# Kernel optimization log

Measured on AMD Instinct MI355X. Metric: run time of the kernel, lower is better.

## Reference

```python
import jax, jax.numpy as jnp
import numpy as np

# Dims: B batch, C=P channels (features per pixel), H*W=N pixels, M ELM models, Q=1 hidden units
M, Q, B, C, H, W_SP = 4, 1, 32, 1024, 28, 28
P = C
N = H * W_SP
EPS = 1e-10


def _lcg_weights(m, n, seed):
    """Deterministic LCG pseudo-random weights, z-score standardized (ELM_AE init)."""
    L = m * n
    a, b, c = L + 2, L + 3, float(L) ** 2
    v = np.zeros(L, dtype=np.float64)
    v[0] = seed + 1.0
    for i in range(1, L):
        v[i] = (a * v[i - 1] + b) % c
    v = (v - v.mean()) / (v.std() + EPS)
    return v.reshape(m, n).astype(np.float32)


def setup_inputs() -> dict:
    key = jax.random.key(0)
    x = jax.random.normal(key, (B, C, H, W_SP), dtype=jnp.float32)
    # One Q x P random input-weight matrix per ELM model, seed = model * (Q * P)
    Wm = jnp.stack([jnp.asarray(_lcg_weights(Q, P, model * (Q * P))) for model in range(M)])  # [M, Q, P]
    return {"x": x, "Wm": Wm}


def reference(x, Wm):
    b, c, h, w = x.shape
    # _norm('l2', ...): per-channel L2 normalization over (h, w), as F.normalize(dim=(1,2))
    norms = jnp.linalg.norm(x.reshape(b, c, h * w), axis=-1)[:, :, None, None]  # [B, C, 1, 1]
    xn = x / jnp.maximum(norms, EPS)
    X = xn.reshape(b, c, h * w)  # meta activation map per sample: [B, P, N]
    # ELM-AE hidden layer, batched over (sample, model): g = sigmoid(W @ X)
    G = jax.nn.sigmoid(jnp.einsum('mqp,bpn->bmqn', Wm, X))  # [B, M, Q, N]
    # fit_AE: output weights beta = pinv(g^T) @ X^T  -> [Q, P]
    pinvGt = jnp.linalg.pinv(jnp.swapaxes(G, -1, -2))       # [B, M, Q, N]
    beta = jnp.einsum('bmqn,bpn->bmqp', pinvGt, X)          # [B, M, Q, P]
    # sum over the M models; Q == 1 so flatten (Q, P) -> Q*P features
    feats = beta.sum(axis=1).reshape(b, -1)                 # [B, Q*P]
    return jnp.nan_to_num(feats)
```

## Files before the change

### kernel.cpp

```cpp
#include <hip/hip_runtime.h>
#include <math.h>

#define BATCH 32
#define CH    1024
#define NPix  784
#define MMOD  4
#define NPC   32
#define PPC   32
#define T2    832

__device__ __forceinline__ float wave_reduce(float s) {
    #pragma unroll
    for (int off = 32; off; off >>= 1) s += __shfl_down(s, off, 64);
    return s;
}

__device__ __forceinline__ float dpp_wave_sum(float v) {
    int x;
    x = __builtin_amdgcn_update_dpp(0, __builtin_bit_cast(int, v), 0x111, 0xf, 0xf, true);
    v += __builtin_bit_cast(float, x);
    x = __builtin_amdgcn_update_dpp(0, __builtin_bit_cast(int, v), 0x112, 0xf, 0xf, true);
    v += __builtin_bit_cast(float, x);
    x = __builtin_amdgcn_update_dpp(0, __builtin_bit_cast(int, v), 0x114, 0xf, 0xf, true);
    v += __builtin_bit_cast(float, x);
    x = __builtin_amdgcn_update_dpp(0, __builtin_bit_cast(int, v), 0x118, 0xf, 0xf, true);
    v += __builtin_bit_cast(float, x);
    x = __builtin_amdgcn_update_dpp(0, __builtin_bit_cast(int, v), 0x142, 0xa, 0xf, true);
    v += __builtin_bit_cast(float, x);
    x = __builtin_amdgcn_update_dpp(0, __builtin_bit_cast(int, v), 0x143, 0xc, 0xf, true);
    v += __builtin_bit_cast(float, x);
    return v;
}

__global__ __launch_bounds__(T2) void k_nz(const float* __restrict__ x,
                                           const float* __restrict__ Wm,
                                           float* __restrict__ inv_norm,
                                           float* __restrict__ zpart) {
    __shared__ float sq_l[PPC * 13];
    __shared__ float4 wl4[PPC];
    const int blk = blockIdx.x;
    const int b  = blk >> 5;
    const int pc = blk & (NPC - 1);
    const int t = threadIdx.x;
    const int wv = t >> 6, lane = t & 63;
    const bool act = (t < NPix);
    const float* xb = x + ((size_t)b * CH + (size_t)pc * PPC) * NPix;
    const float* xp = xb + (act ? t : 0);

    float xv[PPC];
    #pragma unroll
    for (int pp = 0; pp < PPC; pp++) xv[pp] = xp[(size_t)pp * NPix];
    if (!act) {
        #pragma unroll
        for (int pp = 0; pp < PPC; pp++) xv[pp] = 0.f;
    }

    #pragma unroll
    for (int pp = 0; pp < PPC; pp++) {
        float s = dpp_wave_sum(xv[pp] * xv[pp]);
        if (lane == 63) sq_l[pp * 13 + wv] = s;
    }
    __syncthreads();

    if (t < PPC) {
        float s = 0.f;
        #pragma unroll
        for (int w = 0; w < 13; w++) s += sq_l[t * 13 + w];
        const float inv = 1.f / fmaxf(sqrtf(s), 1e-10f);
        const int p = pc * PPC + t;
        inv_norm[b * CH + p] = inv;
        float4 w4;
        w4.x = Wm[0 * CH + p] * inv;
        w4.y = Wm[1 * CH + p] * inv;
        w4.z = Wm[2 * CH + p] * inv;
        w4.w = Wm[3 * CH + p] * inv;
        wl4[t] = w4;
    }
    __syncthreads();

    if (act) {
        float a0 = 0.f, a1 = 0.f, a2 = 0.f, a3 = 0.f;
        #pragma unroll
        for (int pp = 0; pp < PPC; pp++) {
            float4 w = wl4[pp];
            a0 += w.x * xv[pp];
            a1 += w.y * xv[pp];
            a2 += w.z * xv[pp];
            a3 += w.w * xv[pp];
        }
        size_t base = ((size_t)blk * MMOD) * NPix + t;
        zpart[base]            = a0;
        zpart[base + NPix]     = a1;
        zpart[base + 2 * NPix] = a2;
        zpart[base + 3 * NPix] = a3;
    }
}

__global__ __launch_bounds__(T2) void k_gh(const float* __restrict__ zpart,
                                           float* __restrict__ h) {
    __shared__ float red[13][MMOD];
    __shared__ float s2s[MMOD];
    const int b = blockIdx.x;
    const int t = threadIdx.x;
    const int wv = t >> 6, lane = t & 63;
    const bool act = (t < NPix);

    float g[MMOD];
    #pragma unroll
    for (int m = 0; m < MMOD; m++) {
        float z = 0.f;
        if (act) {
            #pragma unroll 8
            for (int pc = 0; pc < NPC; pc++)
                z += zpart[(((size_t)b * NPC + pc) * MMOD + m) * NPix + t];
        }
        g[m] = act ? 1.f / (1.f + expf(-z)) : 0.f;
    }
    #pragma unroll
    for (int m = 0; m < MMOD; m++) {
        float s = wave_reduce(g[m] * g[m]);
        if (lane == 0) red[wv][m] = s;
    }
    __syncthreads();
    if (t < MMOD) {
        float s = 0.f;
        #pragma unroll
        for (int w = 0; w < 13; w++) s += red[w][t];
        s2s[t] = fmaxf(s, 1e-30f);
    }
    __syncthreads();
    if (act) {
        float hv = 0.f;
        #pragma unroll
        for (int m = 0; m < MMOD; m++) hv += g[m] / s2s[m];
        h[(size_t)b * NPix + t] = hv;
    }
}

__global__ __launch_bounds__(256) void k_out(const float* __restrict__ x,
                                             const float* __restrict__ h,
                                             const float* __restrict__ inv_norm,
                                             float* __restrict__ out) {
    const int r = blockIdx.x * 4 + (threadIdx.x >> 6);
    const int lane = threadIdx.x & 63;
    const int b = r >> 10;
    const float4* x4 = (const float4*)(x + (size_t)r * NPix);
    const float4* h4 = (const float4*)(h + (size_t)b * NPix);
    float s = 0.f;
    #pragma unroll
    for (int i = 0; i < 3; i++) {
        float4 xv = x4[i * 64 + lane];
        float4 hv = h4[i * 64 + lane];
        s += xv.x*hv.x + xv.y*hv.y + xv.z*hv.z + xv.w*hv.w;
    }
    if (lane < 4) {
        float4 xv = x4[192 + lane];
        float4 hv = h4[192 + lane];
        s += xv.x*hv.x + xv.y*hv.y + xv.z*hv.z + xv.w*hv.w;
    }
    s = wave_reduce(s);
    if (lane == 0) {
        float v = s * inv_norm[r];
        if (!(v == v)) v = 0.f;
        v = fminf(fmaxf(v, -3.402823466e+38f), 3.402823466e+38f);
        out[r] = v;
    }
}

extern "C" void kernel_launch(void* const* d_in, const int* in_sizes, int n_in,
                              void* d_out, int out_size, void* d_ws, size_t ws_size,
                              hipStream_t stream) {
    const float* x  = (const float*)d_in[0];
    const float* Wm = (const float*)d_in[1];
    float* out = (float*)d_out;
    float* wsf = (float*)d_ws;

    float* inv_norm = wsf;
    float* zpart    = inv_norm + BATCH * CH;
    float* h        = zpart + (size_t)BATCH * NPC * MMOD * NPix;

    k_nz<<<BATCH * NPC, T2, 0, stream>>>(x, Wm, inv_norm, zpart);
    k_gh<<<BATCH, T2, 0, stream>>>(zpart, h);
    k_out<<<BATCH * CH / 4, 256, 0, stream>>>(x, h, inv_norm, out);
}
```

Measured before the change: 182.5 us.

## Vectorize first pass with float4 and split hidden-layer reduction across models

The first kernel now gives each block 16 channels instead of 32, which doubles the block count. It uses 256 threads that each load float4 pixels, so loads are wider and the per-thread register footprint changes. The middle stage is split so one block handles each (batch, model) pair instead of each batch. That raises the block count from 32 to 128 for the zpart reduction, but the number of partial sums per pixel doubles to 64. A small extra kernel combines the per-model g and its squared norm into h, which adds one launch and an intermediate buffer round-trip.

```diff
diff --git a/kernel.cpp b/kernel.cpp
--- a/kernel.cpp
+++ b/kernel.cpp
@@ -5,8 +5,10 @@
 #define CH    1024
 #define NPix  784
 #define MMOD  4
-#define NPC   32
-#define PPC   32
+#define NPC   64
+#define PPC   16
+#define K1B   256
+#define NF4   196
 #define T2    832
 
 __device__ __forceinline__ float wave_reduce(float s) {
@@ -32,40 +34,36 @@
     return v;
 }
 
-__global__ __launch_bounds__(T2) void k_nz(const float* __restrict__ x,
-                                           const float* __restrict__ Wm,
-                                           float* __restrict__ inv_norm,
-                                           float* __restrict__ zpart) {
-    __shared__ float sq_l[PPC * 13];
+__global__ __launch_bounds__(K1B) void k_nz(const float* __restrict__ x,
+                                            const float* __restrict__ Wm,
+                                            float* __restrict__ inv_norm,
+                                            float* __restrict__ zpart) {
+    __shared__ float sq_l[PPC][4];
     __shared__ float4 wl4[PPC];
     const int blk = blockIdx.x;
-    const int b  = blk >> 5;
+    const int b  = blk >> 6;
     const int pc = blk & (NPC - 1);
     const int t = threadIdx.x;
     const int wv = t >> 6, lane = t & 63;
-    const bool act = (t < NPix);
-    const float* xb = x + ((size_t)b * CH + (size_t)pc * PPC) * NPix;
-    const float* xp = xb + (act ? t : 0);
+    const bool act = (t < NF4);
+    const float4* xb4 = (const float4*)(x + ((size_t)b * CH + (size_t)pc * PPC) * NPix);
+    const int tt = act ? t : 0;
 
-    float xv[PPC];
+    float4 xv[PPC];
     #pragma unroll
-    for (int pp = 0; pp < PPC; pp++) xv[pp] = xp[(size_t)pp * NPix];
-    if (!act) {
-        #pragma unroll
-        for (int pp = 0; pp < PPC; pp++) xv[pp] = 0.f;
-    }
+    for (int pp = 0; pp < PPC; pp++) xv[pp] = xb4[pp * NF4 + tt];
 
     #pragma unroll
     for (int pp = 0; pp < PPC; pp++) {
-        float s = dpp_wave_sum(xv[pp] * xv[pp]);
-        if (lane == 63) sq_l[pp * 13 + wv] = s;
+        float4 v = xv[pp];
+        float s = act ? (v.x*v.x + v.y*v.y + v.z*v.z + v.w*v.w) : 0.f;
+        s = dpp_wave_sum(s);
+        if (lane == 63) sq_l[pp][wv] = s;
     }
     __syncthreads();
 
     if (t < PPC) {
-        float s = 0.f;
-        #pragma unroll
-        for (int w = 0; w < 13; w++) s += sq_l[t * 13 + w];
+        const float s = sq_l[t][0] + sq_l[t][1] + sq_l[t][2] + sq_l[t][3];
         const float inv = 1.f / fmaxf(sqrtf(s), 1e-10f);
         const int p = pc * PPC + t;
         inv_norm[b * CH + p] = inv;
@@ -79,60 +77,64 @@
     __syncthreads();
 
     if (act) {
-        float a0 = 0.f, a1 = 0.f, a2 = 0.f, a3 = 0.f;
+        float4 a0 = {0,0,0,0}, a1 = {0,0,0,0}, a2 = {0,0,0,0}, a3 = {0,0,0,0};
         #pragma unroll
         for (int pp = 0; pp < PPC; pp++) {
-            float4 w = wl4[pp];
-            a0 += w.x * xv[pp];
-            a1 += w.y * xv[pp];
-            a2 += w.z * xv[pp];
-            a3 += w.w * xv[pp];
+            const float4 w = wl4[pp];
+            const float4 v = xv[pp];
+            a0.x += w.x*v.x; a0.y += w.x*v.y; a0.z += w.x*v.z; a0.w += w.x*v.w;
+            a1.x += w.y*v.x; a1.y += w.y*v.y; a1.z += w.y*v.z; a1.w += w.y*v.w;
+            a2.x += w.z*v.x; a2.y += w.z*v.y; a2.z += w.z*v.z; a2.w += w.z*v.w;
+            a3.x += w.w*v.x; a3.y += w.w*v.y; a3.z += w.w*v.z; a3.w += w.w*v.w;
         }
-        size_t base = ((size_t)blk * MMOD) * NPix + t;
-        zpart[base]            = a0;
-        zpart[base + NPix]     = a1;
-        zpart[base + 2 * NPix] = a2;
-        zpart[base + 3 * NPix] = a3;
+        float4* zp = (float4*)(zpart + ((size_t)blk * MMOD) * NPix);
+        zp[0 * NF4 + t] = a0;
+        zp[1 * NF4 + t] = a1;
+        zp[2 * NF4 + t] = a2;
+        zp[3 * NF4 + t] = a3;
     }
 }
 
 __global__ __launch_bounds__(T2) void k_gh(const float* __restrict__ zpart,
-                                           float* __restrict__ h) {
-    __shared__ float red[13][MMOD];
-    __shared__ float s2s[MMOD];
-    const int b = blockIdx.x;
+                                           float* __restrict__ g_out,
+                                           float* __restrict__ s2g) {
+    __shared__ float red[13];
+    const int blk = blockIdx.x;
+    const int b = blk >> 2;
+    const int m = blk & 3;
     const int t = threadIdx.x;
     const int wv = t >> 6, lane = t & 63;
     const bool act = (t < NPix);
 
-    float g[MMOD];
-    #pragma unroll
-    for (int m = 0; m < MMOD; m++) {
-        float z = 0.f;
-        if (act) {
-            #pragma unroll 8
-            for (int pc = 0; pc < NPC; pc++)
-                z += zpart[(((size_t)b * NPC + pc) * MMOD + m) * NPix + t];
-        }
-        g[m] = act ? 1.f / (1.f + expf(-z)) : 0.f;
+    float z = 0.f;
+    if (act) {
+        #pragma unroll 8
+        for (int pc = 0; pc < NPC; pc++)
+            z += zpart[(((size_t)(b * NPC + pc)) * MMOD + m) * NPix + t];
     }
-    #pragma unroll
-    for (int m = 0; m < MMOD; m++) {
-        float s = wave_reduce(g[m] * g[m]);
-        if (lane == 0) red[wv][m] = s;
+    const float g = act ? 1.f / (1.f + expf(-z)) : 0.f;
+    float s = wave_reduce(g * g);
+    if (lane == 0) red[wv] = s;
+    __syncthreads();
+    if (t == 0) {
+        float ss = 0.f;
+        #pragma unroll
+        for (int w = 0; w < 13; w++) ss += red[w];
+        s2g[blk] = fmaxf(ss, 1e-30f);
     }
-    __syncthreads();
-    if (t < MMOD) {
-        float s = 0.f;
-        #pragma unroll
-        for (int w = 0; w < 13; w++) s += red[w][t];
-        s2s[t] = fmaxf(s, 1e-30f);
-    }
-    __syncthreads();
-    if (act) {
+    if (act) g_out[(size_t)blk * NPix + t] = g;
+}
+
+__global__ __launch_bounds__(T2) void k_h(const float* __restrict__ g_out,
+                                          const float* __restrict__ s2g,
+                                          float* __restrict__ h) {
+    const int b = blockIdx.x;
+    const int t = threadIdx.x;
+    if (t < NPix) {
         float hv = 0.f;
         #pragma unroll
-        for (int m = 0; m < MMOD; m++) hv += g[m] / s2s[m];
+        for (int m = 0; m < MMOD; m++)
+            hv += g_out[(size_t)(b * MMOD + m) * NPix + t] / s2g[b * MMOD + m];
         h[(size_t)b * NPix + t] = hv;
     }
 }
@@ -177,9 +179,12 @@
 
     float* inv_norm = wsf;
     float* zpart    = inv_norm + BATCH * CH;
-    float* h        = zpart + (size_t)BATCH * NPC * MMOD * NPix;
+    float* g_out    = zpart + (size_t)BATCH * NPC * MMOD * NPix;
+    float* s2g      = g_out + (size_t)BATCH * MMOD * NPix;
+    float* h        = s2g + BATCH * MMOD;
 
-    k_nz<<<BATCH * NPC, T2, 0, stream>>>(x, Wm, inv_norm, zpart);
-    k_gh<<<BATCH, T2, 0, stream>>>(zpart, h);
+    k_nz<<<BATCH * NPC, K1B, 0, stream>>>(x, Wm, inv_norm, zpart);
+    k_gh<<<BATCH * MMOD, T2, 0, stream>>>(zpart, g_out, s2g);
+    k_h<<<BATCH, T2, 0, stream>>>(g_out, s2g, h);
     k_out<<<BATCH * CH / 4, 256, 0, stream>>>(x, h, inv_norm, out);
 }
```

Measured after the change: 176.1 us. 3.5% less time.
